# Kernel tuning notes

Measured on AMD Instinct MI355X. Metric: run time of the kernel, lower is better.

The kernel has to match this reference:

```python
import jax, jax.numpy as jnp
import numpy as np

B, T, F, H = 1024, 100, 64, 256


def _unif(key, shape, stdv):
    return jax.random.uniform(key, shape, jnp.float32, -stdv, stdv)


def setup_inputs() -> dict:
    key = jax.random.key(0)
    ks = jax.random.split(key, 20)
    X = jax.random.normal(ks[0], (B, T, F), jnp.float32)
    missing_mask = jnp.round(jax.random.uniform(ks[1], (B, T, F), jnp.float32))
    deltas = jax.random.uniform(ks[2], (B, T, F), jnp.float32)
    s_h = 1.0 / np.sqrt(H)
    s_f = 1.0 / np.sqrt(F)
    return {
        "X": X, "missing_mask": missing_mask, "deltas": deltas,
        # TemporalDecay h: W [H,F], b [H] (stdv = 1/sqrt(out=H))
        "W_dh": _unif(ks[3], (H, F), s_h), "b_dh": _unif(ks[4], (H,), s_h),
        # TemporalDecay x (diag): W [F,F], b [F]
        "W_dx": _unif(ks[5], (F, F), s_f), "b_dx": _unif(ks[6], (F,), s_f),
        # hist_reg: Linear(H -> F)
        "W_hist": _unif(ks[7], (F, H), s_h), "b_hist": _unif(ks[8], (F,), s_h),
        # feat_reg: W [F,F] masked by (1 - I), b [F]
        "W_feat": _unif(ks[9], (F, F), s_f), "b_feat": _unif(ks[10], (F,), s_f),
        # weight_combine: Linear(2F -> F)
        "W_comb": _unif(ks[11], (F, 2 * F), 1.0 / np.sqrt(2 * F)),
        "b_comb": _unif(ks[12], (F,), 1.0 / np.sqrt(2 * F)),
        # LSTMCell(2F -> H): gates order i,f,g,o
        "W_ih": _unif(ks[13], (4 * H, 2 * F), s_h), "b_ih": _unif(ks[14], (4 * H,), s_h),
        "W_hh": _unif(ks[15], (4 * H, H), s_h), "b_hh": _unif(ks[16], (4 * H,), s_h),
    }


def _masked_mae(inp, tgt, mask):
    return jnp.sum(jnp.abs(inp - tgt) * mask) / (jnp.sum(mask) + 1e-9)


def _rits(X, missing_mask, deltas, W_dh, b_dh, W_dx, b_dx, W_hist, b_hist,
          W_feat, b_feat, W_comb, b_comb, W_ih, b_ih, W_hh, b_hh):
    f = X.shape[-1]
    w_dx_diag = jnp.diag(W_dx)                       # diag TemporalDecay: W * eye
    W_feat_m = W_feat * (1.0 - jnp.eye(f, dtype=W_feat.dtype))

    def step(carry, xt):
        h, c, rec_loss, rec_mae = carry
        x, m, d = xt                                  # each [B, F]
        gamma_h = jnp.exp(-jax.nn.relu(d @ W_dh.T + b_dh))   # [B, H]
        gamma_x = jnp.exp(-jax.nn.relu(d * w_dx_diag + b_dx))  # [B, F]
        h = h * gamma_h
        x_h = h @ W_hist.T + b_hist
        rec_loss = rec_loss + _masked_mae(x_h, x, m)
        x_c = m * x + (1.0 - m) * x_h
        z_h = x_c @ W_feat_m.T + b_feat
        rec_loss = rec_loss + _masked_mae(z_h, x, m)
        alpha = jax.nn.sigmoid(jnp.concatenate([gamma_x, m], axis=1) @ W_comb.T + b_comb)
        c_h = alpha * z_h + (1.0 - alpha) * x_h
        rec_mae = rec_mae + _masked_mae(c_h, x, m)
        rec_loss = rec_loss + rec_mae                 # faithful to source (cumulative MAE added)
        c_c = m * x + (1.0 - m) * c_h
        inputs = jnp.concatenate([c_c, m], axis=1)    # [B, 2F]
        gates = inputs @ W_ih.T + b_ih + h @ W_hh.T + b_hh
        i_g, f_g, g_g, o_g = jnp.split(gates, 4, axis=1)
        c = jax.nn.sigmoid(f_g) * c + jax.nn.sigmoid(i_g) * jnp.tanh(g_g)
        h = jax.nn.sigmoid(o_g) * jnp.tanh(c)
        return (h, c, rec_loss, rec_mae), c_h

    b = X.shape[0]
    hsz = W_hh.shape[1]
    init = (jnp.zeros((b, hsz), X.dtype), jnp.zeros((b, hsz), X.dtype),
            jnp.asarray(0.0, X.dtype), jnp.asarray(0.0, X.dtype))
    xs = (jnp.swapaxes(X, 0, 1), jnp.swapaxes(missing_mask, 0, 1), jnp.swapaxes(deltas, 0, 1))
    (h, c, rec_loss, rec_mae), ests = jax.lax.scan(step, init, xs)
    estimations = jnp.swapaxes(ests, 0, 1)            # [B, T, F]
    imputed = missing_mask * X + (1.0 - missing_mask) * estimations
    seq_len = X.shape[1]
    return imputed, rec_mae / seq_len, rec_loss / (seq_len * 3)


def reference(X, missing_mask, deltas, W_dh, b_dh, W_dx, b_dx, W_hist, b_hist,
              W_feat, b_feat, W_comb, b_comb, W_ih, b_ih, W_hh, b_hh):
    return _rits(X, missing_mask, deltas, W_dh, b_dh, W_dx, b_dx, W_hist, b_hist,
                 W_feat, b_feat, W_comb, b_comb, W_ih, b_ih, W_hh, b_hh)
```

## Files before the change

### kernel.cpp

```cpp
#include <hip/hip_runtime.h>
#include <hip/hip_bf16.h>


#define Bz 1024
#define Tz 100
#define Fz 64
#define Hz 256
#define GROUPS 64
#define SIBS 4
#define RPB 16

typedef __attribute__((ext_vector_type(8))) short short8;
typedef __attribute__((ext_vector_type(4))) float floatx4;
typedef __hip_bfloat16 bf16;
typedef unsigned long long u64;

#define MFMA16(a, b, c) __builtin_amdgcn_mfma_f32_16x16x32_bf16((a), (b), (c), 0, 0, 0)

__device__ __forceinline__ float sigmf(float x) { return 1.0f / (1.0f + __expf(-x)); }
__device__ __forceinline__ float tanhfast(float x) { return 2.0f / (1.0f + __expf(-2.0f * x)) - 1.0f; }


__global__ void rits_convert(const float* __restrict__ Wdh, const float* __restrict__ Wdx,
                             const float* __restrict__ Whist, const float* __restrict__ Wfeat,
                             const float* __restrict__ Wcomb, const float* __restrict__ Wih,
                             const float* __restrict__ Whh, bf16* __restrict__ wsbf,
                             float* __restrict__ wdxd, unsigned int* __restrict__ flagsArr) {
    int idx = blockIdx.x * blockDim.x + threadIdx.x;
    if (idx < 4096) flagsArr[idx] = 0u;
    if (idx < 64) wdxd[idx] = Wdx[idx * 65];
    if (idx >= 438272) return;
    float v;
    if (idx < 16384) v = Wdh[idx];
    else if (idx < 32768) v = Whist[idx - 16384];
    else if (idx < 36864) { int i = idx - 32768; v = ((i >> 6) == (i & 63)) ? 0.0f : Wfeat[i]; }
    else if (idx < 45056) v = Wcomb[idx - 36864];
    else {
        int i = idx - 45056;
        int e = i & 7, q = (i >> 3) & 3, l = (i >> 5) & 15, g = (i >> 9) & 3, w = (i >> 11) & 15;
        int s = i >> 15;
        int n = g * 256 + w * 16 + l;
        v = (s < 4) ? Wih[n * 128 + s * 32 + q * 8 + e] : Whh[n * 256 + (s - 4) * 32 + q * 8 + e];
    }
    wsbf[idx] = __float2bfloat16(v);
}

__global__ __launch_bounds__(1024, 4) void rits_main(
    const float* __restrict__ X, const float* __restrict__ Mm, const float* __restrict__ Dd,
    const float* __restrict__ b_dh, const float* __restrict__ b_dx,
    const float* __restrict__ b_hist, const float* __restrict__ b_feat,
    const float* __restrict__ b_comb, const float* __restrict__ b_ih,
    const float* __restrict__ b_hh,
    const bf16* __restrict__ Wdh, const bf16* __restrict__ Whist,
    const bf16* __restrict__ Wfeatm, const bf16* __restrict__ Wcomb,
    const bf16* __restrict__ Wp5,
    const float* __restrict__ wdxd, float* __restrict__ lossbuf,
    unsigned int* __restrict__ flags, u64* __restrict__ pub, float* __restrict__ out) {
    __shared__ __align__(16) bf16 lw_hist[64 * 264];
    __shared__ __align__(16) bf16 lw_comb[64 * 136];
    __shared__ __align__(16) bf16 lw_feat[64 * 72];
    __shared__ __align__(16) bf16 lw_dh[64 * 72];
    __shared__ __align__(16) bf16 sh_hbf[RPB * 264];
    __shared__ __align__(16) float sh_x[RPB * 64];
    __shared__ __align__(16) float sh_m[RPB * 64];
    __shared__ __align__(16) bf16 sh_dbf2[RPB * 72];
    __shared__ __align__(16) bf16 sh_xcbf[RPB * 72];
    __shared__ __align__(16) bf16 sh_gmbf[RPB * 136];
    __shared__ __align__(16) bf16 sh_inbf[RPB * 136];
    __shared__ __align__(16) float sh_alpha[RPB * 68];
    __shared__ __align__(16) float sh_gam[RPB * 68];
    __shared__ __align__(16) float sh_g[4 * 16 * 66];
    __shared__ __align__(16) float sh_c[64 * 16];
    __shared__ float sh_lred[16];
    __shared__ float sh_msum[16];

    const int tid = threadIdx.x;
    const int lane = tid & 63;
    const int wid = tid >> 6;
    const int l16 = lane & 15;
    const int q = lane >> 4;
    const int j = blockIdx.x & 3;
    const int grp = blockIdx.x >> 2;
    const int b0 = grp * RPB;

    for (int i = tid; i < 64 * 256; i += 1024) lw_hist[(i >> 8) * 264 + (i & 255)] = Whist[i];
    for (int i = tid; i < 64 * 128; i += 1024) lw_comb[(i >> 7) * 136 + (i & 127)] = Wcomb[i];
    for (int i = tid; i < 64 * 64; i += 1024) {
        lw_feat[(i >> 6) * 72 + (i & 63)] = Wfeatm[i];
        lw_dh[(i >> 6) * 72 + (i & 63)] = Wdh[(j * 64 + (i >> 6)) * 64 + (i & 63)];
    }
    for (int i = tid; i < 64 * 16; i += 1024) sh_c[i] = 0.0f;
    for (int i = tid; i < RPB * 264; i += 1024) sh_hbf[i] = (bf16)0.0f;

    const int gate = wid >> 2;
    const int ct = wid & 3;
    const int nrow = gate * 256 + j * 64 + ct * 16 + l16;
    short8 wfrag[12];
#pragma unroll
    for (int s = 0; s < 12; ++s)
        wfrag[s] = *(const short8*)(Wp5 + (size_t)s * 32768 + (j * 4 + ct) * 2048 + gate * 512 +
                                    l16 * 32 + q * 8);
    const float bgate = b_ih[nrow] + b_hh[nrow];

    const float wdxf = wdxd[lane];
    const float bdxf = b_dx[lane];
    const int ca = wid * 16 + l16;
    const int colF = (wid - 4) * 16 + l16;
    const int colg = (wid - 8) * 16 + l16;
    float bc2 = 0.f, bhl = 0.f, bft = 0.f, bdl = 0.f;
    if (wid < 4) bc2 = b_comb[ca];
    else if (wid < 8) { bhl = b_hist[colF]; bft = b_feat[colF]; }
    else if (wid < 12) bdl = b_dh[j * 64 + colg];

    const size_t g0 = (size_t)(b0 + wid) * Tz * Fz + lane;
    float xv = X[g0], mv = Mm[g0], dv = Dd[g0];

    __syncthreads();

    {
        u64* pub0 = pub + (size_t)grp * 2 * 1024;
        if (tid < 256) {
            int col = tid >> 2, qq = tid & 3;
            __hip_atomic_store(pub0 + (size_t)(j * 64 + col) * 4 + qq, 0ull, __ATOMIC_RELAXED,
                               __HIP_MEMORY_SCOPE_AGENT);
        }
        asm volatile("s_waitcnt vmcnt(0)" ::: "memory");
        if (tid < 256 && lane == 0)
            __hip_atomic_store(&flags[((grp * 4 + j) * 4 + wid) * 4], 1u, __ATOMIC_RELAXED,
                               __HIP_MEMORY_SCOPE_AGENT);
    }

    for (int t = 0; t < Tz; ++t) {
        u64* pubt = pub + ((size_t)grp * 2 + (t & 1)) * 1024;

        {
            const int row = wid, f = lane;
            sh_x[row * 64 + f] = xv;
            sh_m[row * 64 + f] = mv;
            float gx = __expf(-fmaxf(dv * wdxf + bdxf, 0.0f));
            sh_gmbf[row * 136 + f] = __float2bfloat16(gx);
            bf16 mb = __float2bfloat16(mv);
            sh_gmbf[row * 136 + 64 + f] = mb;
            sh_inbf[row * 136 + 64 + f] = mb;
            float v0 = mv;
#pragma unroll
            for (int off = 32; off; off >>= 1) v0 += __shfl_xor(v0, off, 64);
            if (lane == 0) sh_msum[wid] = v0;
        }
        if (t + 1 < Tz) {
            size_t g = g0 + (size_t)(t + 1) * Fz;
            xv = X[g]; mv = Mm[g]; dv = Dd[g];
        }
        if (tid < 12) {
            int sidx = tid >> 2;
            int sib = sidx + (sidx >= j);
            int w = tid & 3;
            const unsigned target = (unsigned)(t + 1);
            unsigned it = 0;
            while (__hip_atomic_load(&flags[((grp * 4 + sib) * 4 + w) * 4], __ATOMIC_RELAXED,
                                     __HIP_MEMORY_SCOPE_AGENT) < target) {
                __builtin_amdgcn_s_sleep(1);
                if (++it > (1u << 22)) break;
            }
        }
        __syncthreads();

        if (tid < 768) {
            int sidx = tid >> 8;
            int sib = sidx + (sidx >= j);
            int c = sib * 64 + ((tid >> 2) & 63);
            int qq = tid & 3;
            u64 v = __hip_atomic_load(pubt + (size_t)c * 4 + qq, __ATOMIC_RELAXED,
                                      __HIP_MEMORY_SCOPE_AGENT);
            unsigned short* hb = (unsigned short*)sh_hbf;
#pragma unroll
            for (int r = 0; r < 4; ++r) hb[(qq * 4 + r) * 264 + c] = (unsigned short)(v >> (16 * r));
        }
        __syncthreads();

        floatx4 acc5 = {0.f, 0.f, 0.f, 0.f};
        float xh[4];
        float l1 = 0.f, l2 = 0.f, l3 = 0.f;
        if (wid >= 4 && wid < 8) {
            floatx4 acc = {0.f, 0.f, 0.f, 0.f};
#pragma unroll
            for (int kb = 0; kb < 8; ++kb) {
                short8 a = *(const short8*)(sh_hbf + l16 * 264 + kb * 32 + q * 8);
                short8 b = *(const short8*)(lw_hist + colF * 264 + kb * 32 + q * 8);
                acc = MFMA16(a, b, acc);
            }
#pragma unroll
            for (int r = 0; r < 4; ++r) {
                int row = q * 4 + r;
                xh[r] = acc[r] + bhl;
                float xx = sh_x[row * 64 + colF], mm = sh_m[row * 64 + colF];
                l1 += fabsf(xh[r] - xx) * mm;
                float xc = mm * xx + (1.0f - mm) * xh[r];
                sh_xcbf[row * 72 + colF] = __float2bfloat16(xc);
            }
        } else {
            if (wid < 4) {
                floatx4 acca = {0.f, 0.f, 0.f, 0.f};
#pragma unroll
                for (int kb = 0; kb < 4; ++kb) {
                    short8 a = *(const short8*)(sh_gmbf + l16 * 136 + kb * 32 + q * 8);
                    short8 b = *(const short8*)(lw_comb + ca * 136 + kb * 32 + q * 8);
                    acca = MFMA16(a, b, acca);
                }
#pragma unroll
                for (int r = 0; r < 4; ++r) sh_alpha[(q * 4 + r) * 68 + ca] = sigmf(acca[r] + bc2);
            }
#pragma unroll
            for (int s = 2; s < 4; ++s) {
                short8 a = *(const short8*)(sh_inbf + l16 * 136 + s * 32 + q * 8);
                acc5 = MFMA16(a, wfrag[s], acc5);
            }
#pragma unroll
            for (int s = 4; s < 12; ++s) {
                short8 a = *(const short8*)(sh_hbf + l16 * 264 + (s - 4) * 32 + q * 8);
                acc5 = MFMA16(a, wfrag[s], acc5);
            }
        }
        if (t + 1 < Tz) sh_dbf2[wid * 72 + lane] = __float2bfloat16(dv);
        __syncthreads();

        if (wid >= 4 && wid < 8) {
            floatx4 accz = {0.f, 0.f, 0.f, 0.f};
            {
                short8 a = *(const short8*)(sh_xcbf + l16 * 72 + q * 8);
                accz = MFMA16(a, *(const short8*)(lw_feat + colF * 72 + q * 8), accz);
                a = *(const short8*)(sh_xcbf + l16 * 72 + 32 + q * 8);
                accz = MFMA16(a, *(const short8*)(lw_feat + colF * 72 + 32 + q * 8), accz);
            }
#pragma unroll
            for (int r = 0; r < 4; ++r) {
                int row = q * 4 + r;
                float xx = sh_x[row * 64 + colF], mm = sh_m[row * 64 + colF];
                float z = accz[r] + bft;
                l2 += fabsf(z - xx) * mm;
                float al = sh_alpha[row * 68 + colF];
                float ch = al * z + (1.0f - al) * xh[r];
                l3 += fabsf(ch - xx) * mm;
                float imp = mm * xx + (1.0f - mm) * ch;
                if (wid - 4 == j) out[((size_t)(b0 + row) * Tz + t) * Fz + colF] = imp;
                sh_inbf[row * 136 + colF] = __float2bfloat16(imp);
            }
            float v1 = l1, v2 = l2, v3 = l3;
#pragma unroll
            for (int off = 32; off; off >>= 1) {
                v1 += __shfl_xor(v1, off, 64);
                v2 += __shfl_xor(v2, off, 64);
                v3 += __shfl_xor(v3, off, 64);
            }
            if (lane == 0) {
                sh_lred[(wid - 4) * 4 + 0] = v1;
                sh_lred[(wid - 4) * 4 + 1] = v2;
                sh_lred[(wid - 4) * 4 + 2] = v3;
            }
        } else if (wid >= 8 && wid < 12 && t + 1 < Tz) {
            short8 a0 = *(const short8*)(sh_dbf2 + l16 * 72 + q * 8);
            short8 a1 = *(const short8*)(sh_dbf2 + l16 * 72 + 32 + q * 8);
            short8 w0 = *(const short8*)(lw_dh + colg * 72 + q * 8);
            short8 w1 = *(const short8*)(lw_dh + colg * 72 + 32 + q * 8);
            floatx4 acc = {0.f, 0.f, 0.f, 0.f};
            acc = MFMA16(a0, w0, acc);
            acc = MFMA16(a1, w1, acc);
#pragma unroll
            for (int r = 0; r < 4; ++r)
                sh_gam[(q * 4 + r) * 68 + colg] = __expf(-fmaxf(acc[r] + bdl, 0.0f));
        }
        __syncthreads();

        {
#pragma unroll
            for (int s = 0; s < 2; ++s) {
                short8 a = *(const short8*)(sh_inbf + l16 * 136 + s * 32 + q * 8);
                acc5 = MFMA16(a, wfrag[s], acc5);
            }
#pragma unroll
            for (int r = 0; r < 4; ++r) {
                float v = acc5[r] + bgate;
                float tv = (gate == 2) ? tanhfast(v) : sigmf(v);
                sh_g[(gate * 16 + q * 4 + r) * 66 + ct * 16 + l16] = tv;
            }
        }
        __syncthreads();

        if (tid < 256) {
            int col = tid >> 2, q2 = tid & 3;
            int gcol = j * 64 + col;
            float4 cv = *(float4*)(sh_c + col * 16 + q2 * 4);
            float cc[4] = {cv.x, cv.y, cv.z, cv.w};
            u64 pk = 0;
#pragma unroll
            for (int r = 0; r < 4; ++r) {
                int row = q2 * 4 + r;
                float Ig = sh_g[(0 * 16 + row) * 66 + col];
                float Fg = sh_g[(1 * 16 + row) * 66 + col];
                float Gg = sh_g[(2 * 16 + row) * 66 + col];
                float Og = sh_g[(3 * 16 + row) * 66 + col];
                float c = Fg * cc[r] + Ig * Gg;
                cc[r] = c;
                if (t + 1 < Tz) {
                    float h = Og * tanhfast(c);
                    float hd = h * sh_gam[row * 68 + col];
                    bf16 hb = __float2bfloat16(hd);
                    sh_hbf[row * 264 + gcol] = hb;
                    pk |= (u64)(*(unsigned short*)&hb) << (16 * r);
                }
            }
            *(float4*)(sh_c + col * 16 + q2 * 4) = (float4){cc[0], cc[1], cc[2], cc[3]};
            if (t + 1 < Tz) {
                u64* pubn = pub + ((size_t)grp * 2 + ((t + 1) & 1)) * 1024;
                __hip_atomic_store(pubn + (size_t)gcol * 4 + q2, pk, __ATOMIC_RELAXED,
                                   __HIP_MEMORY_SCOPE_AGENT);
            }
        }
        if (tid < 256 && t + 1 < Tz) {
            asm volatile("s_waitcnt vmcnt(0)" ::: "memory");
            if (lane == 0)
                __hip_atomic_store(&flags[((grp * 4 + j) * 4 + wid) * 4], (unsigned)(t + 2),
                                   __ATOMIC_RELAXED, __HIP_MEMORY_SCOPE_AGENT);
        }
        if (tid == 256 && ((t & 3) == j)) {
            float s0 = 0.0f;
#pragma unroll
            for (int i = 0; i < 16; ++i) s0 += sh_msum[i];
            float* lb = lossbuf + ((size_t)grp * Tz + t) * 4;
            lb[0] = s0;
            lb[1] = sh_lred[0] + sh_lred[4] + sh_lred[8] + sh_lred[12];
            lb[2] = sh_lred[1] + sh_lred[5] + sh_lred[9] + sh_lred[13];
            lb[3] = sh_lred[2] + sh_lred[6] + sh_lred[10] + sh_lred[14];
        }
        __syncthreads();
    }
}

__global__ void rits_finalize(const float* __restrict__ lossbuf, float* __restrict__ out) {
    __shared__ float m1[Tz], m2[Tz], m3[Tz];
    int t = threadIdx.x;
    if (t < Tz) {
        float s0 = 0.0f, s1 = 0.0f, s2 = 0.0f, s3 = 0.0f;
        for (int g = 0; g < GROUPS; ++g) {
            const float* lb = lossbuf + ((size_t)g * Tz + t) * 4;
            s0 += lb[0]; s1 += lb[1]; s2 += lb[2]; s3 += lb[3];
        }
        float inv = 1.0f / (s0 + 1e-9f);
        m1[t] = s1 * inv; m2[t] = s2 * inv; m3[t] = s3 * inv;
    }
    __syncthreads();
    if (t == 0) {
        float rm = 0.0f, rl = 0.0f;
        for (int i = 0; i < Tz; ++i) {
            rl += m1[i]; rl += m2[i]; rm += m3[i]; rl += rm;
        }
        out[(size_t)Bz * Tz * Fz] = rm / (float)Tz;
        out[(size_t)Bz * Tz * Fz + 1] = rl / (3.0f * (float)Tz);
    }
}

extern "C" void kernel_launch(void* const* d_in, const int* in_sizes, int n_in,
                              void* d_out, int out_size, void* d_ws, size_t ws_size,
                              hipStream_t stream) {
    const float* X = (const float*)d_in[0];
    const float* Mm = (const float*)d_in[1];
    const float* Dd = (const float*)d_in[2];
    const float* Wdh = (const float*)d_in[3];
    const float* b_dh = (const float*)d_in[4];
    const float* Wdx = (const float*)d_in[5];
    const float* b_dx = (const float*)d_in[6];
    const float* Whist = (const float*)d_in[7];
    const float* b_hist = (const float*)d_in[8];
    const float* Wfeat = (const float*)d_in[9];
    const float* b_feat = (const float*)d_in[10];
    const float* Wcomb = (const float*)d_in[11];
    const float* b_comb = (const float*)d_in[12];
    const float* Wih = (const float*)d_in[13];
    const float* b_ih = (const float*)d_in[14];
    const float* Whh = (const float*)d_in[15];
    const float* b_hh = (const float*)d_in[16];
    float* out = (float*)d_out;

    bf16* wsbf = (bf16*)d_ws;
    float* wdxd = (float*)((char*)d_ws + 876544);
    float* lossbuf = (float*)((char*)d_ws + 876800);
    unsigned int* flags = (unsigned int*)((char*)d_ws + 979200);
    u64* pub = (u64*)((char*)d_ws + 995584);

    rits_convert<<<1712, 256, 0, stream>>>(Wdh, Wdx, Whist, Wfeat, Wcomb, Wih, Whh, wsbf, wdxd,
                                           flags);
    rits_main<<<GROUPS * SIBS, 1024, 0, stream>>>(
        X, Mm, Dd, b_dh, b_dx, b_hist, b_feat, b_comb, b_ih, b_hh, wsbf + 0, wsbf + 16384,
        wsbf + 32768, wsbf + 36864, wsbf + 45056, wdxd, lossbuf, flags, pub, out);
    rits_finalize<<<1, 128, 0, stream>>>(lossbuf, out);
}
```

Measured before the change: 973.8 us.

## Fold sibling h exchange into end-of-step barrier and drop extra syncs

Restructures the per-step cross-block handshake. Each of the 768 non-publishing threads now spins on its own producer's flag and pulls the sibling h values directly into shared memory at the end of step t, instead of 12 threads spinning and then taking two extra __syncthreads at the start of the next step. Staging of the next timestep's x/m/delta also moves to the end of the step, with a double-buffered mask-sum slot, and the initial zeroing and flag=1 publication are dropped. The aim is fewer block barriers per step and overlap of the flag wait with other tail work, at the cost of more threads spinning on global atomics. The step-0 pub buffer is no longer zeroed, but step 0 never reads it because the initial h is zero.

Result: slower. 1.090 ms (+12.0%).

```diff
diff --git a/kernel.cpp b/kernel.cpp
--- a/kernel.cpp
+++ b/kernel.cpp
@@ -72,7 +72,7 @@
     __shared__ __align__(16) float sh_g[4 * 16 * 66];
     __shared__ __align__(16) float sh_c[64 * 16];
     __shared__ float sh_lred[16];
-    __shared__ float sh_msum[16];
+    __shared__ float sh_msum[2][16];
 
     const int tid = threadIdx.x;
     const int lane = tid & 63;
@@ -115,69 +115,26 @@
     const size_t g0 = (size_t)(b0 + wid) * Tz * Fz + lane;
     float xv = X[g0], mv = Mm[g0], dv = Dd[g0];
 
+    {
+        sh_x[wid * 64 + lane] = xv;
+        sh_m[wid * 64 + lane] = mv;
+        float gx = __expf(-fmaxf(dv * wdxf + bdxf, 0.0f));
+        sh_gmbf[wid * 136 + lane] = __float2bfloat16(gx);
+        bf16 mb = __float2bfloat16(mv);
+        sh_gmbf[wid * 136 + 64 + lane] = mb;
+        sh_inbf[wid * 136 + 64 + lane] = mb;
+        float v0 = mv;
+#pragma unroll
+        for (int off = 32; off; off >>= 1) v0 += __shfl_xor(v0, off, 64);
+        if (lane == 0) sh_msum[0][wid] = v0;
+    }
+    {
+        size_t g = g0 + (size_t)Fz;
+        xv = X[g]; mv = Mm[g]; dv = Dd[g];
+    }
     __syncthreads();
 
-    {
-        u64* pub0 = pub + (size_t)grp * 2 * 1024;
-        if (tid < 256) {
-            int col = tid >> 2, qq = tid & 3;
-            __hip_atomic_store(pub0 + (size_t)(j * 64 + col) * 4 + qq, 0ull, __ATOMIC_RELAXED,
-                               __HIP_MEMORY_SCOPE_AGENT);
-        }
-        asm volatile("s_waitcnt vmcnt(0)" ::: "memory");
-        if (tid < 256 && lane == 0)
-            __hip_atomic_store(&flags[((grp * 4 + j) * 4 + wid) * 4], 1u, __ATOMIC_RELAXED,
-                               __HIP_MEMORY_SCOPE_AGENT);
-    }
-
     for (int t = 0; t < Tz; ++t) {
-        u64* pubt = pub + ((size_t)grp * 2 + (t & 1)) * 1024;
-
-        {
-            const int row = wid, f = lane;
-            sh_x[row * 64 + f] = xv;
-            sh_m[row * 64 + f] = mv;
-            float gx = __expf(-fmaxf(dv * wdxf + bdxf, 0.0f));
-            sh_gmbf[row * 136 + f] = __float2bfloat16(gx);
-            bf16 mb = __float2bfloat16(mv);
-            sh_gmbf[row * 136 + 64 + f] = mb;
-            sh_inbf[row * 136 + 64 + f] = mb;
-            float v0 = mv;
-#pragma unroll
-            for (int off = 32; off; off >>= 1) v0 += __shfl_xor(v0, off, 64);
-            if (lane == 0) sh_msum[wid] = v0;
-        }
-        if (t + 1 < Tz) {
-            size_t g = g0 + (size_t)(t + 1) * Fz;
-            xv = X[g]; mv = Mm[g]; dv = Dd[g];
-        }
-        if (tid < 12) {
-            int sidx = tid >> 2;
-            int sib = sidx + (sidx >= j);
-            int w = tid & 3;
-            const unsigned target = (unsigned)(t + 1);
-            unsigned it = 0;
-            while (__hip_atomic_load(&flags[((grp * 4 + sib) * 4 + w) * 4], __ATOMIC_RELAXED,
-                                     __HIP_MEMORY_SCOPE_AGENT) < target) {
-                __builtin_amdgcn_s_sleep(1);
-                if (++it > (1u << 22)) break;
-            }
-        }
-        __syncthreads();
-
-        if (tid < 768) {
-            int sidx = tid >> 8;
-            int sib = sidx + (sidx >= j);
-            int c = sib * 64 + ((tid >> 2) & 63);
-            int qq = tid & 3;
-            u64 v = __hip_atomic_load(pubt + (size_t)c * 4 + qq, __ATOMIC_RELAXED,
-                                      __HIP_MEMORY_SCOPE_AGENT);
-            unsigned short* hb = (unsigned short*)sh_hbf;
-#pragma unroll
-            for (int r = 0; r < 4; ++r) hb[(qq * 4 + r) * 264 + c] = (unsigned short)(v >> (16 * r));
-        }
-        __syncthreads();
-
         floatx4 acc5 = {0.f, 0.f, 0.f, 0.f};
         float xh[4];
         float l1 = 0.f, l2 = 0.f, l3 = 0.f;
@@ -314,23 +271,60 @@
                 u64* pubn = pub + ((size_t)grp * 2 + ((t + 1) & 1)) * 1024;
                 __hip_atomic_store(pubn + (size_t)gcol * 4 + q2, pk, __ATOMIC_RELAXED,
                                    __HIP_MEMORY_SCOPE_AGENT);
-            }
-        }
-        if (tid < 256 && t + 1 < Tz) {
-            asm volatile("s_waitcnt vmcnt(0)" ::: "memory");
-            if (lane == 0)
-                __hip_atomic_store(&flags[((grp * 4 + j) * 4 + wid) * 4], (unsigned)(t + 2),
-                                   __ATOMIC_RELAXED, __HIP_MEMORY_SCOPE_AGENT);
+                asm volatile("s_waitcnt vmcnt(0)" ::: "memory");
+                if (lane == 0)
+                    __hip_atomic_store(&flags[((grp * 4 + j) * 4 + wid) * 4], (unsigned)(t + 2),
+                                       __ATOMIC_RELAXED, __HIP_MEMORY_SCOPE_AGENT);
+            }
+        }
+        if (t + 1 < Tz) {
+            sh_x[wid * 64 + lane] = xv;
+            sh_m[wid * 64 + lane] = mv;
+            float gx = __expf(-fmaxf(dv * wdxf + bdxf, 0.0f));
+            sh_gmbf[wid * 136 + lane] = __float2bfloat16(gx);
+            bf16 mb = __float2bfloat16(mv);
+            sh_gmbf[wid * 136 + 64 + lane] = mb;
+            sh_inbf[wid * 136 + 64 + lane] = mb;
+            float v0 = mv;
+#pragma unroll
+            for (int off = 32; off; off >>= 1) v0 += __shfl_xor(v0, off, 64);
+            if (lane == 0) sh_msum[(t + 1) & 1][wid] = v0;
+            if (t + 2 < Tz) {
+                size_t g = g0 + (size_t)(t + 2) * Fz;
+                xv = X[g]; mv = Mm[g]; dv = Dd[g];
+            }
         }
         if (tid == 256 && ((t & 3) == j)) {
             float s0 = 0.0f;
 #pragma unroll
-            for (int i = 0; i < 16; ++i) s0 += sh_msum[i];
+            for (int i = 0; i < 16; ++i) s0 += sh_msum[t & 1][i];
             float* lb = lossbuf + ((size_t)grp * Tz + t) * 4;
             lb[0] = s0;
             lb[1] = sh_lred[0] + sh_lred[4] + sh_lred[8] + sh_lred[12];
             lb[2] = sh_lred[1] + sh_lred[5] + sh_lred[9] + sh_lred[13];
             lb[3] = sh_lred[2] + sh_lred[6] + sh_lred[10] + sh_lred[14];
+        }
+        if (tid >= 256 && t + 1 < Tz) {
+            int idx = tid - 256;
+            int sidx = idx >> 8;
+            int sib = sidx + (sidx >= j);
+            int cl = (idx >> 2) & 63;
+            int c = sib * 64 + cl;
+            int qq = idx & 3;
+            const unsigned target = (unsigned)(t + 2);
+            const unsigned int* fp = &flags[((grp * 4 + sib) * 4 + (cl >> 4)) * 4];
+            unsigned it = 0;
+            while (__hip_atomic_load(fp, __ATOMIC_RELAXED, __HIP_MEMORY_SCOPE_AGENT) < target) {
+                __builtin_amdgcn_s_sleep(1);
+                if (++it > (1u << 22)) break;
+            }
+            asm volatile("" ::: "memory");
+            const u64* pubt1 = pub + ((size_t)grp * 2 + ((t + 1) & 1)) * 1024;
+            u64 v = __hip_atomic_load(pubt1 + (size_t)c * 4 + qq, __ATOMIC_RELAXED,
+                                      __HIP_MEMORY_SCOPE_AGENT);
+            unsigned short* hb = (unsigned short*)sh_hbf;
+#pragma unroll
+            for (int r = 0; r < 4; ++r) hb[(qq * 4 + r) * 264 + c] = (unsigned short)(v >> (16 * r));
         }
         __syncthreads();
     }
```
